# Kernel tuning notes

Hardware: AMD Instinct MI355X
Metric: run time of the kernel (lower is better)

Reference implementation:

```python
import jax, jax.numpy as jnp
import numpy as np

GROUPS = 32
EPS = 1e-5


def group_norm(x, scale, bias):
    b, c, h, w = x.shape
    xg = x.reshape(b, GROUPS, c // GROUPS, h, w)
    mean = jnp.mean(xg, axis=(2, 3, 4), keepdims=True)
    var = jnp.var(xg, axis=(2, 3, 4), keepdims=True)
    xn = (xg - mean) * jax.lax.rsqrt(var + EPS)
    xn = xn.reshape(b, c, h, w)
    return xn * scale[None, :, None, None] + bias[None, :, None, None]


def conv1x1(x, w, b):
    # x: [b,c,h,w], w: [out,in] -> [b,out,h,w]
    return jnp.einsum('bchw,oc->bohw', x, w) + b[None, :, None, None]


def setup_inputs() -> dict:
    key = jax.random.key(0)
    ks = jax.random.split(key, 8)
    B, C, H, W = 4, 512, 64, 64
    s = 1.0 / np.sqrt(C)
    return {
        'x': jax.random.normal(ks[0], (B, C, H, W), jnp.float32),
        'norm_scale': jnp.ones((C,), jnp.float32),
        'norm_bias': jnp.zeros((C,), jnp.float32),
        'wq': jax.random.normal(ks[1], (C, C), jnp.float32) * s,
        'bq': jnp.zeros((C,), jnp.float32),
        'wk': jax.random.normal(ks[2], (C, C), jnp.float32) * s,
        'bk': jnp.zeros((C,), jnp.float32),
        'wv': jax.random.normal(ks[3], (C, C), jnp.float32) * s,
        'bv': jnp.zeros((C,), jnp.float32),
        'wo': jax.random.normal(ks[4], (C, C), jnp.float32) * s,
        'bo': jnp.zeros((C,), jnp.float32),
    }


def reference(x, norm_scale, norm_bias, wq, bq, wk, bk, wv, bv, wo, bo):
    b, c, h, w = x.shape
    hn = group_norm(x, norm_scale, norm_bias)
    q = conv1x1(hn, wq, bq)  # [b,c,h,w]
    k = conv1x1(hn, wk, bk)
    v = conv1x1(hn, wv, bv)
    n = h * w
    q = q.reshape(b, c, n).transpose(0, 2, 1)  # [b,n,c]
    k = k.reshape(b, c, n)                     # [b,c,n]
    v = v.reshape(b, c, n).transpose(0, 2, 1)  # [b,n,c]
    scale = jnp.asarray(c, x.dtype) ** -0.5
    attn = jax.nn.softmax(jnp.einsum('bic,bcj->bij', q, k) * scale, axis=-1)
    out = jnp.einsum('bij,bjc->bic', attn, v)  # [b,n,c]
    out = out.transpose(0, 2, 1).reshape(b, c, h, w)
    return x + conv1x1(out, wo, bo)
```

## Files before the change

### kernel.cpp

```cpp
#include <hip/hip_runtime.h>
#include <math.h>

#define B_ 4
#define C_ 512
#define N_ 4096
#define NG 32

typedef __attribute__((ext_vector_type(4))) float f32x4;
typedef __attribute__((ext_vector_type(8))) short bf16x8;
typedef __attribute__((ext_vector_type(8))) unsigned short u16x8;
typedef __attribute__((ext_vector_type(4))) unsigned short u16x4;

__device__ __forceinline__ unsigned short f2bf(float f){
  unsigned u = __float_as_uint(f);
  return (unsigned short)((u + 0x7fffu + ((u >> 16) & 1u)) >> 16);
}
__device__ __forceinline__ float bf2f(unsigned short h){
  return __uint_as_float(((unsigned)h) << 16);
}

__global__ __launch_bounds__(256) void gn_stats_k(const float* __restrict__ x, float* __restrict__ stats){
  int bg = blockIdx.x;
  const float4* xp = (const float4*)(x + (size_t)bg * 65536);
  float s = 0.f, ss = 0.f;
  for (int i = threadIdx.x; i < 16384; i += 256){
    float4 v = xp[i];
    s  += v.x + v.y + v.z + v.w;
    ss += v.x*v.x + v.y*v.y + v.z*v.z + v.w*v.w;
  }
  __shared__ float ls[256], lq[256];
  ls[threadIdx.x] = s; lq[threadIdx.x] = ss;
  __syncthreads();
  for (int o = 128; o > 0; o >>= 1){
    if (threadIdx.x < o){ ls[threadIdx.x] += ls[threadIdx.x+o]; lq[threadIdx.x] += lq[threadIdx.x+o]; }
    __syncthreads();
  }
  if (threadIdx.x == 0){
    float mean = ls[0] * (1.f/65536.f);
    float var  = lq[0] * (1.f/65536.f) - mean*mean;
    stats[bg*2+0] = mean;
    stats[bg*2+1] = rsqrtf(var + 1e-5f);
  }
}

__global__ __launch_bounds__(256) void gn_apply_k(const float* __restrict__ x, const float* __restrict__ stats,
    const float* __restrict__ gam, const float* __restrict__ bet, unsigned short* __restrict__ hn){
  __shared__ unsigned short tile[C_][33];
  int b = blockIdx.y, n0 = blockIdx.x * 32;
  const float* xb = x + (size_t)b * C_ * N_;
  for (int i = threadIdx.x; i < 4096; i += 256){
    int c = i >> 3, j4 = (i & 7) * 4;
    float4 v = *(const float4*)(xb + (size_t)c * N_ + n0 + j4);
    int g = c >> 4;
    float mean = stats[(b*NG+g)*2], rstd = stats[(b*NG+g)*2+1];
    float sc = gam[c] * rstd;
    float bi = bet[c] - mean * sc;
    tile[c][j4+0] = f2bf(v.x*sc+bi);
    tile[c][j4+1] = f2bf(v.y*sc+bi);
    tile[c][j4+2] = f2bf(v.z*sc+bi);
    tile[c][j4+3] = f2bf(v.w*sc+bi);
  }
  __syncthreads();
  for (int i = threadIdx.x; i < 2048; i += 256){
    int cc = (i & 63) * 8, j = i >> 6;
    u16x8 o;
    #pragma unroll
    for (int t = 0; t < 8; t++) o[t] = tile[cc+t][j];
    *(u16x8*)(hn + ((size_t)b*N_ + n0 + j) * C_ + cc) = o;
  }
}

__global__ __launch_bounds__(256) void prep_w_k(const float* __restrict__ wq, const float* __restrict__ wk,
    const float* __restrict__ wv, const float* __restrict__ wo,
    unsigned short* __restrict__ wqkv, unsigned short* __restrict__ wob, float scl){
  int i = blockIdx.x * 256 + threadIdx.x;
  int mat = i >> 16, idx = i & 65535;
  const float* src = (mat==0) ? wq : (mat==1) ? wk : (mat==2) ? wv : wo;
  float s = (mat==0) ? scl : 1.f;
  float4 v = ((const float4*)src)[idx];
  u16x4 o; o[0]=f2bf(v.x*s); o[1]=f2bf(v.y*s); o[2]=f2bf(v.z*s); o[3]=f2bf(v.w*s);
  if (mat < 3) ((u16x4*)wqkv)[mat*65536 + idx] = o;
  else         ((u16x4*)wob)[idx] = o;
}

__global__ __launch_bounds__(256) void prep_b_k(const float* __restrict__ bq, const float* __restrict__ bk,
    const float* __restrict__ bv, float* __restrict__ bqkv, float scl){
  int i = blockIdx.x * 256 + threadIdx.x;
  if (i < 512) bqkv[i] = bq[i] * scl;
  else if (i < 1024) bqkv[i] = bk[i-512];
  else if (i < 1536) bqkv[i] = bv[i-1024];
}

__global__ __launch_bounds__(256) void sm_stats_k(const float* __restrict__ part, float* __restrict__ rsum){
  int i = blockIdx.x * 256 + threadIdx.x;
  const float4* p = (const float4*)(part + (size_t)i * 64);
  float S = 0.f;
  #pragma unroll
  for (int j = 0; j < 16; j++){ float4 v = p[j]; S += v.x + v.y + v.z + v.w; }
  rsum[i] = 1.f / S;
}

template<int BIAS_MODE , bool OUT_BF16, bool RESID, bool EXPSTATS, bool SCALE_ROW>
__global__ __launch_bounds__(512) void gemm_bt_k(
    const unsigned short* __restrict__ A, const unsigned short* __restrict__ Bt,
    void* __restrict__ Cv, const float* __restrict__ bias, const float* __restrict__ resid,
    int Ncols, int K, int lda, int ldb,
    long long sA, long long sB, long long sC, long long sR, float scale,
    float* __restrict__ part, const float* __restrict__ rsum)
{
  const int tid = threadIdx.x;
  const int bz = blockIdx.z;
  A  += (size_t)bz * sA;
  Bt += (size_t)bz * sB;

  const int nwg = gridDim.x * gridDim.y;
  const int wg  = blockIdx.y * gridDim.x + blockIdx.x;
  const int swz = (wg & 7) * (nwg >> 3) + (wg >> 3);
  const int bx = swz % gridDim.x, by = swz / gridDim.x;

  const int tn = bx * 128, tm = by * 256;
  const int Mtot = gridDim.y * 256;
  __shared__ unsigned short lA[2][256*32];
  __shared__ unsigned short lB[2][128*32];
  const int wave = tid >> 6, lane = tid & 63;
  const int wm = (wave >> 1) * 64, wn = (wave & 1) * 64;
  f32x4 acc[4][4] = {};

  const unsigned short* Abase = A + (size_t)tm * lda;
  const unsigned short* Bbase = Bt + (size_t)tn * ldb;

  const int srow = tid >> 2, pch = tid & 3;
  const int sch  = pch ^ ((srow >> 1) & 3);
  const size_t aoff0 = (size_t)srow       * lda + sch*8;
  const size_t aoff1 = (size_t)(srow+128) * lda + sch*8;
  const size_t boff0 = (size_t)srow       * ldb + sch*8;
  const int ldst0 = srow*32       + pch*8;
  const int ldst1 = (srow+128)*32 + pch*8;

  auto issue = [&](int buf, int k0){
    __builtin_amdgcn_global_load_lds((const __attribute__((address_space(1))) unsigned int*)(Abase + aoff0 + k0),
        (__attribute__((address_space(3))) unsigned int*)(&lA[buf][ldst0]), 16, 0, 0);
    __builtin_amdgcn_global_load_lds((const __attribute__((address_space(1))) unsigned int*)(Abase + aoff1 + k0),
        (__attribute__((address_space(3))) unsigned int*)(&lA[buf][ldst1]), 16, 0, 0);
    __builtin_amdgcn_global_load_lds((const __attribute__((address_space(1))) unsigned int*)(Bbase + boff0 + k0),
        (__attribute__((address_space(3))) unsigned int*)(&lB[buf][ldst0]), 16, 0, 0);
  };

  issue(0, 0);
  __syncthreads();
  const int T = K >> 5;
  for (int t = 0; t < T; t++){
    const int cur = t & 1;
    if (t + 1 < T) issue(cur ^ 1, (t + 1) << 5);

    bf16x8 af[4], bfb[4];
    const int lr = lane & 15, q = lane >> 4;
    #pragma unroll
    for (int i = 0; i < 4; i++){
      int row = wm + i*16 + lr;
      af[i]  = *(const bf16x8*)&lA[cur][row*32 + ((q ^ ((row >> 1) & 3)) * 8)];
    }
    #pragma unroll
    for (int j = 0; j < 4; j++){
      int row = wn + j*16 + lr;
      bfb[j] = *(const bf16x8*)&lB[cur][row*32 + ((q ^ ((row >> 1) & 3)) * 8)];
    }
    #pragma unroll
    for (int i = 0; i < 4; i++)
      #pragma unroll
      for (int j = 0; j < 4; j++)
        acc[i][j] = __builtin_amdgcn_mfma_f32_16x16x32_bf16(af[i], bfb[j], acc[i][j], 0, 0, 0);

    __syncthreads();
  }

  const int rr = (lane >> 4) * 4, cl = lane & 15;
  #pragma unroll
  for (int i = 0; i < 4; i++){
    #pragma unroll
    for (int r = 0; r < 4; r++){
      int row = tm + wm + i*16 + rr + r;
      float se = 0.f;
      #pragma unroll
      for (int j = 0; j < 4; j++){
        int col = tn + wn + j*16 + cl;
        float v = acc[i][j][r];
        if (BIAS_MODE == 1) v += bias[col];
        if (BIAS_MODE == 2) v += bias[row];
        v *= scale;
        if (SCALE_ROW) v *= rsum[(size_t)bz * Mtot + row];
        size_t idx = (size_t)bz * sC + (size_t)row * Ncols + col;
        if (RESID) v += resid[(size_t)bz * sR + (size_t)row * Ncols + col];
        if (EXPSTATS){
          unsigned short h = f2bf(__expf(v));
          ((unsigned short*)Cv)[idx] = h;
          se += bf2f(h);
        } else if (OUT_BF16){
          ((unsigned short*)Cv)[idx] = f2bf(v);
        } else {
          ((float*)Cv)[idx] = v;
        }
      }
      if (EXPSTATS){
        #pragma unroll
        for (int o = 1; o < 16; o <<= 1) se += __shfl_xor(se, o);
        if ((lane & 15) == 0)
          part[((size_t)bz * Mtot + row) * 64 + bx*2 + (wave & 1)] = se;
      }
    }
  }
}

__global__ __launch_bounds__(256) void transpose_v_k(const unsigned short* __restrict__ QKV, unsigned short* __restrict__ Vt){
  __shared__ unsigned short t[64][72];
  int b = blockIdx.z, c0 = blockIdx.x * 64, n0 = blockIdx.y * 64;
  int tid = threadIdx.x;
  for (int i = tid; i < 512; i += 256){
    int n = i >> 3, cc = (i & 7) * 8;
    u16x8 v = *(const u16x8*)&QKV[((size_t)b*N_ + n0 + n)*1536 + 1024 + c0 + cc];
    #pragma unroll
    for (int j = 0; j < 8; j++) t[cc+j][n] = v[j];
  }
  __syncthreads();
  for (int i = tid; i < 512; i += 256){
    int c = i >> 3, nn = (i & 7) * 8;
    u16x8 o;
    #pragma unroll
    for (int j = 0; j < 8; j++) o[j] = t[c][nn+j];
    *(u16x8*)&Vt[((size_t)b*C_ + c0 + c)*N_ + n0 + nn] = o;
  }
}

__global__ __launch_bounds__(256) void softmax_k(unsigned short* __restrict__ SP){
  size_t row = blockIdx.x;
  u16x8* sp = (u16x8*)(SP + row * 4096);
  const int t = threadIdx.x;
  u16x8 h0 = sp[t], h1 = sp[t + 256];
  float v[16];
  #pragma unroll
  for (int j = 0; j < 8; j++){ v[j] = bf2f(h0[j]); v[8+j] = bf2f(h1[j]); }
  float m = -3.0e38f;
  #pragma unroll
  for (int j = 0; j < 16; j++) m = fmaxf(m, v[j]);
  #pragma unroll
  for (int o = 32; o > 0; o >>= 1) m = fmaxf(m, __shfl_xor(m, o));
  __shared__ float red[4], red2[4];
  if ((t & 63) == 0) red[t >> 6] = m;
  __syncthreads();
  m = fmaxf(fmaxf(red[0], red[1]), fmaxf(red[2], red[3]));
  float s = 0.f;
  #pragma unroll
  for (int j = 0; j < 16; j++){ float e = __expf(v[j] - m); v[j] = e; s += e; }
  #pragma unroll
  for (int o = 32; o > 0; o >>= 1) s += __shfl_xor(s, o);
  if ((t & 63) == 0) red2[t >> 6] = s;
  __syncthreads();
  s = red2[0] + red2[1] + red2[2] + red2[3];
  float inv = 1.0f / s;
  u16x8 o0, o1;
  #pragma unroll
  for (int j = 0; j < 8; j++){ o0[j] = f2bf(v[j] * inv); o1[j] = f2bf(v[8+j] * inv); }
  sp[t] = o0; sp[t + 256] = o1;
}

extern "C" void kernel_launch(void* const* d_in, const int* in_sizes, int n_in,
                              void* d_out, int out_size, void* d_ws, size_t ws_size,
                              hipStream_t stream)
{
  (void)in_sizes; (void)n_in; (void)out_size;
  const float* x   = (const float*)d_in[0];
  const float* gam = (const float*)d_in[1];
  const float* bet = (const float*)d_in[2];
  const float* wq  = (const float*)d_in[3];
  const float* bq  = (const float*)d_in[4];
  const float* wk  = (const float*)d_in[5];
  const float* bk  = (const float*)d_in[6];
  const float* wv  = (const float*)d_in[7];
  const float* bv  = (const float*)d_in[8];
  const float* wo  = (const float*)d_in[9];
  const float* bo  = (const float*)d_in[10];

  char* ws = (char*)d_ws;
  size_t off = 0;
  auto alloc = [&](size_t bytes)->void*{ void* p = ws + off; off += (bytes + 255) & ~(size_t)255; return p; };
  unsigned short* hn   = (unsigned short*)alloc((size_t)B_*N_*C_*2);
  unsigned short* QKV  = (unsigned short*)alloc((size_t)B_*N_*1536*2);
  unsigned short* Vt   = (unsigned short*)alloc((size_t)B_*C_*N_*2);
  unsigned short* O    = (unsigned short*)alloc((size_t)B_*N_*C_*2);
  unsigned short* wqkv = (unsigned short*)alloc((size_t)3*C_*C_*2);
  unsigned short* wob  = (unsigned short*)alloc((size_t)C_*C_*2);
  float* bqkv          = (float*)alloc(1536*4);
  float* stats         = (float*)alloc((size_t)B_*NG*2*4);
  float* part          = (float*)alloc((size_t)B_*N_*64*4);
  float* rsumb         = (float*)alloc((size_t)B_*N_*4);

  size_t base = off;
  long long avail = (long long)ws_size - (long long)base;
  long long per_row = (long long)N_*2;
  long long rows_ll = avail > 0 ? avail / per_row : 0;
  int rows = (int)(rows_ll > 16384 ? 16384 : rows_ll);
  rows = (rows / 256) * 256;
  if (rows < 256) rows = 256;
  unsigned short* S = (unsigned short*)(ws + base);

  const float scl = 0.044194173824159216f;
  const long long NC  = (long long)N_ * C_;
  const long long CN  = (long long)C_ * N_;
  const long long NN  = (long long)N_ * N_;
  const long long NC3 = (long long)N_ * 1536;

  prep_w_k<<<dim3(1024), 256, 0, stream>>>(wq, wk, wv, wo, wqkv, wob, scl);
  prep_b_k<<<dim3(6),    256, 0, stream>>>(bq, bk, bv, bqkv, scl);

  gn_stats_k<<<dim3(B_*NG), 256, 0, stream>>>(x, stats);
  gn_apply_k<<<dim3(N_/32, B_), 256, 0, stream>>>(x, stats, gam, bet, hn);

  gemm_bt_k<1,true,false,false,false><<<dim3(1536/128, B_*N_/256, 1), 512, 0, stream>>>(
      hn, wqkv, QKV, bqkv, nullptr, 1536, C_, C_, C_, 0,0,0,0, 1.f, nullptr, nullptr);

  transpose_v_k<<<dim3(C_/64, N_/64, B_), 256, 0, stream>>>(QKV, Vt);

  if (rows >= B_*N_){
    gemm_bt_k<0,true,false,true,false><<<dim3(N_/128, N_/256, B_), 512, 0, stream>>>(
        QKV, QKV + 512, S, nullptr, nullptr, N_, C_, 1536, 1536, NC3, NC3, NN, 0, 1.f,
        part, nullptr);
    sm_stats_k<<<dim3(B_*N_/256), 256, 0, stream>>>(part, rsumb);
    gemm_bt_k<0,true,false,false,true><<<dim3(C_/128, N_/256, B_), 512, 0, stream>>>(
        S, Vt, O, nullptr, nullptr, C_, N_, N_, N_, NN, CN, NC, 0, 1.f,
        nullptr, rsumb);
  } else {
    int CH = rows > N_ ? N_ : rows;
    for (int b = 0; b < B_; b++){
      for (int r0 = 0; r0 < N_; r0 += CH){
        int ch = (N_ - r0) < CH ? (N_ - r0) : CH;
        gemm_bt_k<0,true,false,false,false><<<dim3(N_/128, ch/256, 1), 512, 0, stream>>>(
            QKV + ((size_t)b*N_ + r0)*1536, QKV + (size_t)b*N_*1536 + 512, S, nullptr, nullptr,
            N_, C_, 1536, 1536, 0,0,0,0, 1.f, nullptr, nullptr);
        softmax_k<<<dim3(ch), 256, 0, stream>>>(S);
        gemm_bt_k<0,true,false,false,false><<<dim3(C_/128, ch/256, 1), 512, 0, stream>>>(
            S, Vt + (size_t)b*C_*N_, O + ((size_t)b*N_ + r0)*C_, nullptr, nullptr,
            C_, N_, N_, N_, 0,0,0,0, 1.f, nullptr, nullptr);
      }
    }
  }

  gemm_bt_k<2,false,true,false,false><<<dim3(N_/128, C_/256, B_), 512, 0, stream>>>(
      wob, O, (float*)d_out, bo, x, N_, C_, C_, C_, 0, NC, CN, CN, 1.f, nullptr, nullptr);
}
```

Before: 313.1 us.

## Use 4-wave GEMM with 8x4 MFMA tiles and triple-buffered async LDS loads

Adds a new GEMM kernel that uses 256 threads per block, with each wave computing a 128x64 sub-tile (8x4 MFMA accumulators) instead of 64x64. LDS goes from double to triple buffering, with prefetch two K-steps ahead. Synchronisation moves from __syncthreads to explicit vmcnt waits plus s_barrier, and s_setprio is raised around the MFMA block. The aim is more reuse per wave and better overlap of global loads with compute. The cost is higher register pressure and more LDS per block, which may reduce occupancy; the old kernel is kept only for the chunked fallback path.

```diff
diff --git a/kernel.cpp b/kernel.cpp
--- a/kernel.cpp
+++ b/kernel.cpp
@@ -100,8 +100,11 @@
   rsum[i] = 1.f / S;
 }
 
+#define AS1 __attribute__((address_space(1)))
+#define AS3 __attribute__((address_space(3)))
+
 template<int BIAS_MODE , bool OUT_BF16, bool RESID, bool EXPSTATS, bool SCALE_ROW>
-__global__ __launch_bounds__(512) void gemm_bt_k(
+__global__ __launch_bounds__(256, 2) void gemm8_k(
     const unsigned short* __restrict__ A, const unsigned short* __restrict__ Bt,
     void* __restrict__ Cv, const float* __restrict__ bias, const float* __restrict__ resid,
     int Ncols, int K, int lda, int ldb,
@@ -120,71 +123,82 @@
 
   const int tn = bx * 128, tm = by * 256;
   const int Mtot = gridDim.y * 256;
-  __shared__ unsigned short lA[2][256*32];
-  __shared__ unsigned short lB[2][128*32];
+  __shared__ unsigned short lA[3][256*32];
+  __shared__ unsigned short lB[3][128*32];
   const int wave = tid >> 6, lane = tid & 63;
-  const int wm = (wave >> 1) * 64, wn = (wave & 1) * 64;
-  f32x4 acc[4][4] = {};
+  const int wm = (wave >> 1) * 128, wn = (wave & 1) * 64;
+  f32x4 acc[8][4] = {};
 
   const unsigned short* Abase = A + (size_t)tm * lda;
   const unsigned short* Bbase = Bt + (size_t)tn * ldb;
 
-  const int srow = tid >> 2, pch = tid & 3;
-  const int sch  = pch ^ ((srow >> 1) & 3);
-  const size_t aoff0 = (size_t)srow       * lda + sch*8;
-  const size_t aoff1 = (size_t)(srow+128) * lda + sch*8;
-  const size_t boff0 = (size_t)srow       * ldb + sch*8;
-  const int ldst0 = srow*32       + pch*8;
-  const int ldst1 = (srow+128)*32 + pch*8;
+  const int sr = tid >> 2, p = tid & 3;
 
   auto issue = [&](int buf, int k0){
-    __builtin_amdgcn_global_load_lds((const __attribute__((address_space(1))) unsigned int*)(Abase + aoff0 + k0),
-        (__attribute__((address_space(3))) unsigned int*)(&lA[buf][ldst0]), 16, 0, 0);
-    __builtin_amdgcn_global_load_lds((const __attribute__((address_space(1))) unsigned int*)(Abase + aoff1 + k0),
-        (__attribute__((address_space(3))) unsigned int*)(&lA[buf][ldst1]), 16, 0, 0);
-    __builtin_amdgcn_global_load_lds((const __attribute__((address_space(1))) unsigned int*)(Bbase + boff0 + k0),
-        (__attribute__((address_space(3))) unsigned int*)(&lB[buf][ldst0]), 16, 0, 0);
+    #pragma unroll
+    for (int i = 0; i < 4; i++){
+      int row = i*64 + sr;
+      int l = p ^ ((row >> 1) & 3);
+      __builtin_amdgcn_global_load_lds((const AS1 unsigned int*)(Abase + (size_t)row*lda + k0 + l*8),
+          (AS3 unsigned int*)(&lA[buf][row*32 + p*8]), 16, 0, 0);
+    }
+    #pragma unroll
+    for (int j = 0; j < 2; j++){
+      int row = j*64 + sr;
+      int l = p ^ ((row >> 1) & 3);
+      __builtin_amdgcn_global_load_lds((const AS1 unsigned int*)(Bbase + (size_t)row*ldb + k0 + l*8),
+          (AS3 unsigned int*)(&lB[buf][row*32 + p*8]), 16, 0, 0);
+    }
   };
 
+  const int T = K >> 5;
   issue(0, 0);
-  __syncthreads();
-  const int T = K >> 5;
+  issue(1, 32);
+
+  int cur = 0;
   for (int t = 0; t < T; t++){
-    const int cur = t & 1;
-    if (t + 1 < T) issue(cur ^ 1, (t + 1) << 5);
-
-    bf16x8 af[4], bfb[4];
+    if (t < T - 1) { asm volatile("s_waitcnt vmcnt(6)" ::: "memory"); }
+    else           { asm volatile("s_waitcnt vmcnt(0)" ::: "memory"); }
+    __builtin_amdgcn_s_barrier();
+    __builtin_amdgcn_sched_barrier(0);
+
+    bf16x8 af[8], bfb[4];
     const int lr = lane & 15, q = lane >> 4;
     #pragma unroll
-    for (int i = 0; i < 4; i++){
-      int row = wm + i*16 + lr;
-      af[i]  = *(const bf16x8*)&lA[cur][row*32 + ((q ^ ((row >> 1) & 3)) * 8)];
-    }
-    #pragma unroll
-    for (int j = 0; j < 4; j++){
-      int row = wn + j*16 + lr;
-      bfb[j] = *(const bf16x8*)&lB[cur][row*32 + ((q ^ ((row >> 1) & 3)) * 8)];
-    }
-    #pragma unroll
-    for (int i = 0; i < 4; i++)
+    for (int m = 0; m < 8; m++){
+      int row = wm + m*16 + lr;
+      af[m] = *(const bf16x8*)&lA[cur][row*32 + ((q ^ ((row >> 1) & 3)) * 8)];
+    }
+    #pragma unroll
+    for (int n = 0; n < 4; n++){
+      int row = wn + n*16 + lr;
+      bfb[n] = *(const bf16x8*)&lB[cur][row*32 + ((q ^ ((row >> 1) & 3)) * 8)];
+    }
+    if (t + 2 < T){
+      int nb = cur + 2; if (nb >= 3) nb -= 3;
+      issue(nb, (t + 2) << 5);
+    }
+    __builtin_amdgcn_s_setprio(1);
+    #pragma unroll
+    for (int m = 0; m < 8; m++)
       #pragma unroll
-      for (int j = 0; j < 4; j++)
-        acc[i][j] = __builtin_amdgcn_mfma_f32_16x16x32_bf16(af[i], bfb[j], acc[i][j], 0, 0, 0);
-
-    __syncthreads();
+      for (int n = 0; n < 4; n++)
+        acc[m][n] = __builtin_amdgcn_mfma_f32_16x16x32_bf16(af[m], bfb[n], acc[m][n], 0, 0, 0);
+    __builtin_amdgcn_s_setprio(0);
+    cur++; if (cur >= 3) cur = 0;
   }
 
   const int rr = (lane >> 4) * 4, cl = lane & 15;
   #pragma unroll
-  for (int i = 0; i < 4; i++){
+  for (int m = 0; m < 8; m++){
     #pragma unroll
     for (int r = 0; r < 4; r++){
-      int row = tm + wm + i*16 + rr + r;
+      int row = tm + wm + m*16 + rr + r;
       float se = 0.f;
       #pragma unroll
-      for (int j = 0; j < 4; j++){
-        int col = tn + wn + j*16 + cl;
-        float v = acc[i][j][r];
+      for (int n = 0; n < 4; n++){
+        int col = tn + wn + n*16 + cl;
+        float v = acc[m][n][r];
         if (BIAS_MODE == 1) v += bias[col];
         if (BIAS_MODE == 2) v += bias[row];
         v *= scale;
@@ -211,6 +225,92 @@
   }
 }
 
+template<int BIAS_MODE, bool OUT_BF16, bool RESID>
+__global__ __launch_bounds__(512) void gemm_bt_k(
+    const unsigned short* __restrict__ A, const unsigned short* __restrict__ Bt,
+    void* __restrict__ Cv, const float* __restrict__ bias, const float* __restrict__ resid,
+    int Ncols, int K, int lda, int ldb,
+    long long sA, long long sB, long long sC, long long sR, float scale)
+{
+  const int tid = threadIdx.x;
+  const int bz = blockIdx.z;
+  A  += (size_t)bz * sA;
+  Bt += (size_t)bz * sB;
+  const int nwg = gridDim.x * gridDim.y;
+  const int wg  = blockIdx.y * gridDim.x + blockIdx.x;
+  const int swz = (wg & 7) * (nwg >> 3) + (wg >> 3);
+  const int bx = swz % gridDim.x, by = swz / gridDim.x;
+  const int tn = bx * 128, tm = by * 256;
+  __shared__ unsigned short lA[2][256*32];
+  __shared__ unsigned short lB[2][128*32];
+  const int wave = tid >> 6, lane = tid & 63;
+  const int wm = (wave >> 1) * 64, wn = (wave & 1) * 64;
+  f32x4 acc[4][4] = {};
+  const unsigned short* Abase = A + (size_t)tm * lda;
+  const unsigned short* Bbase = Bt + (size_t)tn * ldb;
+  const int srow = tid >> 2, pch = tid & 3;
+  const int sch  = pch ^ ((srow >> 1) & 3);
+  const size_t aoff0 = (size_t)srow       * lda + sch*8;
+  const size_t aoff1 = (size_t)(srow+128) * lda + sch*8;
+  const size_t boff0 = (size_t)srow       * ldb + sch*8;
+  const int ldst0 = srow*32       + pch*8;
+  const int ldst1 = (srow+128)*32 + pch*8;
+  auto issue = [&](int buf, int k0){
+    __builtin_amdgcn_global_load_lds((const AS1 unsigned int*)(Abase + aoff0 + k0),
+        (AS3 unsigned int*)(&lA[buf][ldst0]), 16, 0, 0);
+    __builtin_amdgcn_global_load_lds((const AS1 unsigned int*)(Abase + aoff1 + k0),
+        (AS3 unsigned int*)(&lA[buf][ldst1]), 16, 0, 0);
+    __builtin_amdgcn_global_load_lds((const AS1 unsigned int*)(Bbase + boff0 + k0),
+        (AS3 unsigned int*)(&lB[buf][ldst0]), 16, 0, 0);
+  };
+  issue(0, 0);
+  __syncthreads();
+  const int T = K >> 5;
+  for (int t = 0; t < T; t++){
+    const int cur = t & 1;
+    if (t + 1 < T) issue(cur ^ 1, (t + 1) << 5);
+    bf16x8 af[4], bfb[4];
+    const int lr = lane & 15, q = lane >> 4;
+    #pragma unroll
+    for (int i = 0; i < 4; i++){
+      int row = wm + i*16 + lr;
+      af[i]  = *(const bf16x8*)&lA[cur][row*32 + ((q ^ ((row >> 1) & 3)) * 8)];
+    }
+    #pragma unroll
+    for (int j = 0; j < 4; j++){
+      int row = wn + j*16 + lr;
+      bfb[j] = *(const bf16x8*)&lB[cur][row*32 + ((q ^ ((row >> 1) & 3)) * 8)];
+    }
+    #pragma unroll
+    for (int i = 0; i < 4; i++)
+      #pragma unroll
+      for (int j = 0; j < 4; j++)
+        acc[i][j] = __builtin_amdgcn_mfma_f32_16x16x32_bf16(af[i], bfb[j], acc[i][j], 0, 0, 0);
+    __syncthreads();
+  }
+  const int rr = (lane >> 4) * 4, cl = lane & 15;
+  #pragma unroll
+  for (int i = 0; i < 4; i++){
+    #pragma unroll
+    for (int j = 0; j < 4; j++){
+      int col = tn + wn + j*16 + cl;
+      float cb = (BIAS_MODE == 1) ? bias[col] : 0.f;
+      #pragma unroll
+      for (int r = 0; r < 4; r++){
+        int row = tm + wm + i*16 + rr + r;
+        float v = acc[i][j][r];
+        if (BIAS_MODE == 1) v += cb;
+        if (BIAS_MODE == 2) v += bias[row];
+        v *= scale;
+        size_t idx = (size_t)bz * sC + (size_t)row * Ncols + col;
+        if (RESID) v += resid[(size_t)bz * sR + (size_t)row * Ncols + col];
+        if (OUT_BF16) ((unsigned short*)Cv)[idx] = f2bf(v);
+        else          ((float*)Cv)[idx] = v;
+      }
+    }
+  }
+}
+
 __global__ __launch_bounds__(256) void transpose_v_k(const unsigned short* __restrict__ QKV, unsigned short* __restrict__ Vt){
   __shared__ unsigned short t[64][72];
   int b = blockIdx.z, c0 = blockIdx.x * 64, n0 = blockIdx.y * 64;
@@ -315,17 +415,17 @@
   gn_stats_k<<<dim3(B_*NG), 256, 0, stream>>>(x, stats);
   gn_apply_k<<<dim3(N_/32, B_), 256, 0, stream>>>(x, stats, gam, bet, hn);
 
-  gemm_bt_k<1,true,false,false,false><<<dim3(1536/128, B_*N_/256, 1), 512, 0, stream>>>(
+  gemm8_k<1,true,false,false,false><<<dim3(1536/128, B_*N_/256, 1), 256, 0, stream>>>(
       hn, wqkv, QKV, bqkv, nullptr, 1536, C_, C_, C_, 0,0,0,0, 1.f, nullptr, nullptr);
 
   transpose_v_k<<<dim3(C_/64, N_/64, B_), 256, 0, stream>>>(QKV, Vt);
 
   if (rows >= B_*N_){
-    gemm_bt_k<0,true,false,true,false><<<dim3(N_/128, N_/256, B_), 512, 0, stream>>>(
+    gemm8_k<0,true,false,true,false><<<dim3(N_/128, N_/256, B_), 256, 0, stream>>>(
         QKV, QKV + 512, S, nullptr, nullptr, N_, C_, 1536, 1536, NC3, NC3, NN, 0, 1.f,
         part, nullptr);
     sm_stats_k<<<dim3(B_*N_/256), 256, 0, stream>>>(part, rsumb);
-    gemm_bt_k<0,true,false,false,true><<<dim3(C_/128, N_/256, B_), 512, 0, stream>>>(
+    gemm8_k<0,true,false,false,true><<<dim3(C_/128, N_/256, B_), 256, 0, stream>>>(
         S, Vt, O, nullptr, nullptr, C_, N_, N_, N_, NN, CN, NC, 0, 1.f,
         nullptr, rsumb);
   } else {
@@ -333,17 +433,17 @@
     for (int b = 0; b < B_; b++){
       for (int r0 = 0; r0 < N_; r0 += CH){
         int ch = (N_ - r0) < CH ? (N_ - r0) : CH;
-        gemm_bt_k<0,true,false,false,false><<<dim3(N_/128, ch/256, 1), 512, 0, stream>>>(
+        gemm_bt_k<0,true,false><<<dim3(N_/128, ch/256, 1), 512, 0, stream>>>(
             QKV + ((size_t)b*N_ + r0)*1536, QKV + (size_t)b*N_*1536 + 512, S, nullptr, nullptr,
-            N_, C_, 1536, 1536, 0,0,0,0, 1.f, nullptr, nullptr);
+            N_, C_, 1536, 1536, 0,0,0,0, 1.f);
         softmax_k<<<dim3(ch), 256, 0, stream>>>(S);
-        gemm_bt_k<0,true,false,false,false><<<dim3(C_/128, ch/256, 1), 512, 0, stream>>>(
+        gemm_bt_k<0,true,false><<<dim3(C_/128, ch/256, 1), 512, 0, stream>>>(
             S, Vt + (size_t)b*C_*N_, O + ((size_t)b*N_ + r0)*C_, nullptr, nullptr,
-            C_, N_, N_, N_, 0,0,0,0, 1.f, nullptr, nullptr);
+            C_, N_, N_, N_, 0,0,0,0, 1.f);
       }
     }
   }
 
-  gemm_bt_k<2,false,true,false,false><<<dim3(N_/128, C_/256, B_), 512, 0, stream>>>(
+  gemm8_k<2,false,true,false,false><<<dim3(N_/128, C_/256, B_), 256, 0, stream>>>(
       wob, O, (float*)d_out, bo, x, N_, C_, C_, C_, 0, NC, CN, CN, 1.f, nullptr, nullptr);
 }
```

New measurement: 299.2 us. 4.4% less time.
